# Optimization experiments

Measured on AMD Instinct MI355X. Metric: run time of the kernel, lower is better.

Reference implementation:

```python
import jax, jax.numpy as jnp
import numpy as np

# dims
B, NO, NE = 32, 100, 600          # batch, img objects, img edges
NK, KE, L = 1000, 1000, 8         # kg entities, kg edges, token len
R = 8                              # reasoning-program nodes
H, IMG, LOC = 512, 2048, 5        # hidden, img feat, loc feat
EMB, V, MID, C = 300, 10000, 512, 3000
PAD = 1


def lang_encode(tokens, embed, W, b):
    # masked mean-pool of word embeddings + projection (LanguageEncoder)
    m = (tokens != PAD).astype(jnp.float32)            # [B,N,L]
    e = embed[tokens]                                   # [B,N,L,EMB]
    pooled = (e * m[..., None]).sum(-2) / jnp.maximum(m.sum(-1, keepdims=True), 1.0)
    return jnp.tanh(pooled @ W + b)                     # [B,N,H]


def find_attn(q, k, mask, Wq, Wk, v):
    # Find module: additive attention of program-node queries over key set
    qp = q @ Wq                                         # [B,R,MID]
    kp = k @ Wk                                         # [B,N,MID]
    s = jnp.einsum('brnm,m->brn', jnp.tanh(qp[:, :, None, :] + kp[:, None, :, :]), v)
    if mask is not None:
        s = jnp.where(mask[:, None, :], s, -1e9)
    return jax.nn.softmax(s, axis=-1)                   # [B,R,N] attention maps


def setup_inputs():
    key = jax.random.key(0)
    ks = jax.random.split(key, 30)
    w = lambda i, shp: jax.random.normal(ks[i], shp, jnp.float32) * 0.05
    inp = {
        'img_feat': jax.random.normal(ks[0], (B, NO, IMG), jnp.float32),
        'img_loc': jax.random.uniform(ks[1], (B, NO, LOC), jnp.float32),
        'img_node1_id_list': jax.random.randint(ks[2], (B, NE), 0, NO),
        'img_node2_id_list': jax.random.randint(ks[3], (B, NE), 0, NO),
        'kg_entity': jax.random.randint(ks[4], (B, NK, L), 0, V),
        'kg_e1_ids_list': jax.random.randint(ks[5], (B, KE), 0, NK),
        'kg_e2_ids_list': jax.random.randint(ks[6], (B, KE), 0, NK),
        'kg_edge': jax.random.randint(ks[7], (B, KE, L), 0, V),
        'r_nodes': jax.random.randint(ks[8], (B, R, L), 0, V),
        'r_connects': jax.random.randint(ks[9], (B, R), 0, R),
        'r_type': jax.random.randint(ks[10], (B, R), 0, 3),
        'embed': w(11, (V, EMB)),
        'W_lang': w(12, (EMB, H)), 'b_lang': jnp.zeros((H,), jnp.float32),
        'W_img': w(13, (IMG, H)), 'b_img': jnp.zeros((H,), jnp.float32),
        'W_loc': w(14, (LOC, H)), 'b_loc': jnp.zeros((H,), jnp.float32),
        'W_rel': w(15, (2 * H, H)), 'b_rel': jnp.zeros((H,), jnp.float32),
        'Wq_n': w(16, (H, MID)), 'Wk_n': w(17, (H, MID)), 'v_n': w(18, (MID,)),
        'Wq_e': w(19, (H, MID)), 'Wk_e': w(20, (H, MID)), 'v_e': w(21, (MID,)),
        'W1': w(22, (H, MID)), 'b1': jnp.zeros((MID,), jnp.float32),
        'W2': w(23, (MID, C)), 'b2': jnp.zeros((C,), jnp.float32),
    }
    return inp


def reference(img_feat, img_loc, img_node1_id_list, img_node2_id_list, kg_entity,
              kg_e1_ids_list, kg_e2_ids_list, kg_edge, r_nodes, r_connects, r_type,
              embed, W_lang, b_lang, W_img, b_img, W_loc, b_loc, W_rel, b_rel,
              Wq_n, Wk_n, v_n, Wq_e, Wk_e, v_e, W1, b1, W2, b2):
    # --- image graph features ---
    img_f = img_feat @ W_img + b_img                    # [B,NO,H]
    img_node_feat = img_f + (img_loc @ W_loc + b_loc)
    n1 = jnp.take_along_axis(img_f, img_node1_id_list[..., None], axis=1)  # [B,NE,H]
    n2 = jnp.take_along_axis(img_f, img_node2_id_list[..., None], axis=1)
    img_edge_feat = jnp.concatenate([n1, n2], -1) @ W_rel + b_rel          # [B,NE,H]
    # --- kg graph features ---
    kg_node_feat = lang_encode(kg_entity, embed, W_lang, b_lang)           # [B,NK,H]
    kg_node_mask = jnp.any(kg_entity != PAD, axis=-1)                      # [B,NK]
    kg_edge_feat = lang_encode(kg_edge, embed, W_lang, b_lang)             # [B,KE,H]
    # --- reasoning-program node features ---
    r_feat = lang_encode(r_nodes, embed, W_lang, b_lang)                   # [B,R,H]
    # --- Find over nodes (img + kg entities) ---
    node_keys = jnp.concatenate([img_node_feat, kg_node_feat], axis=1)     # [B,NO+NK,H]
    node_mask = jnp.concatenate([jnp.ones((B, NO), bool), kg_node_mask], axis=1)
    all_map = find_attn(r_feat, node_keys, node_mask, Wq_n, Wk_n, v_n)     # [B,R,NO+NK]
    node_re = jnp.einsum('brn,bnh->brh', all_map, node_keys)               # grounded node feats
    # --- Find over edges (img + kg relations) ---
    edge_keys = jnp.concatenate([img_edge_feat, kg_edge_feat], axis=1)     # [B,NE+KE,H]
    edge_map = find_attn(r_feat, edge_keys, None, Wq_e, Wk_e, v_e)
    edge_ctx = jnp.einsum('brn,bnh->brh', edge_map, edge_keys)
    # --- Reason head on root program node ---
    final = node_re[:, -1] + edge_ctx[:, -1]                               # [B,H]
    return jnp.tanh(final @ W1 + b1) @ W2 + b2                             # [B,C]
```

## Files before the change

kernel.cpp:

```cpp
#include <hip/hip_runtime.h>
#include <hip/hip_bf16.h>
#include <math.h>

#define B_   32
#define NO_  100
#define NE_  600
#define NK_  1000
#define KE_  1000
#define L_   8
#define R_   8
#define H_   512
#define IMG_ 2048
#define LOC_ 5
#define EMB_ 300
#define MID_ 512
#define C_   3000
#define PAD_ 1

#define NN_  (NO_ + NK_)
#define NEK_ (NE_ + KE_)

typedef __attribute__((ext_vector_type(8))) short bf16x8;
typedef __attribute__((ext_vector_type(4))) float f32x4;

__device__ __forceinline__ float4 ldf4(const float* p) { return *(const float4*)p; }

__device__ __forceinline__ float bf2f(short s) {
    unsigned u = ((unsigned)(unsigned short)s) << 16;
    float f; __builtin_memcpy(&f, &u, 4); return f;
}
__device__ __forceinline__ short f2bf(float f) {
    unsigned u; __builtin_memcpy(&u, &f, 4);
    u = (u + 0x7fffu + ((u >> 16) & 1u)) >> 16;
    return (short)u;
}

__global__ __launch_bounds__(256) void wprep_kernel(
    const float* __restrict__ W, short* __restrict__ Wp, int K, int KS)
{
    int idx = blockIdx.x * 256 + threadIdx.x;
    int total = 4 * KS * 4 * 128;
    if (idx >= total) return;
    int nl = idx & 127;
    int kg = (idx >> 7) & 3;
    int t  = idx >> 9;
    int ks = t % KS;
    int nb = t / KS;
    int n = nb * 128 + nl;
    short o[8];
#pragma unroll
    for (int j = 0; j < 8; ++j) {
        int k = ks * 32 + kg * 8 + j;
        o[j] = (k < K) ? f2bf(W[(long)k * H_ + n]) : (short)0;
    }
    *(uint4*)&Wp[(long)idx * 8] = *(uint4*)o;
}

__global__ __launch_bounds__(256) void cvt_bf16_kernel(
    const float* __restrict__ src, short* __restrict__ dst, long n)
{
    long i = ((long)blockIdx.x * 256 + threadIdx.x) * 8;
    if (i >= n) return;
    float4 a = ldf4(src + i), b = ldf4(src + i + 4);
    short o[8] = { f2bf(a.x), f2bf(a.y), f2bf(a.z), f2bf(a.w),
                   f2bf(b.x), f2bf(b.y), f2bf(b.z), f2bf(b.w) };
    *(uint4*)&dst[i] = *(uint4*)o;
}

__global__ __launch_bounds__(256) void pool_kernel(
    const int* __restrict__ tokens, int tok_stride, int tok_off,
    const short* __restrict__ embed_bf, short* __restrict__ pooled,
    float* __restrict__ maskout, int nrows)
{
    __shared__ int   toks[32][8];
    __shared__ float rinv[32];
    int tid = threadIdx.x, base = blockIdx.x * 32;
    {
        int r = tid >> 3, t = tid & 7;
        int i = base + r;
        toks[r][t] = (i < nrows) ? tokens[tok_off + (long)i * tok_stride + t] : PAD_;
    }
    __syncthreads();
    if (tid < 32) {
        int c = 0;
#pragma unroll
        for (int t = 0; t < 8; ++t) c += (toks[tid][t] != PAD_);
        rinv[tid] = 1.0f / fmaxf((float)c, 1.0f);
        int i = base + tid;
        if (maskout && i < nrows) maskout[i] = (c > 0) ? 1.0f : 0.0f;
    }
    __syncthreads();

    for (int task = tid; task < 32 * 40; task += 256) {
        int r = task / 40, kg = task - r * 40;
        float s[8] = {0.f,0.f,0.f,0.f,0.f,0.f,0.f,0.f};
        if (kg < 38) {
#pragma unroll
            for (int t = 0; t < 8; ++t) {
                int tok = toks[r][t];
                if (tok != PAD_) {
                    bf16x8 e = *(const bf16x8*)&embed_bf[(long)tok * EMB_ + kg * 8];
#pragma unroll
                    for (int j = 0; j < 8; ++j) s[j] += bf2f(e[j]);
                }
            }
        }
        float iv = rinv[r];
        short o[8];
#pragma unroll
        for (int j = 0; j < 8; ++j) {
            float v = s[j] * iv;
            if (kg == 37 && j >= 4) v = 0.f;
            o[j] = f2bf(v);
        }
        *(uint4*)&pooled[(long)(base + r) * 320 + kg * 8] = *(uint4*)o;
    }
}

template<int OUTF32>
__global__ __launch_bounds__(256) void keys_gemm_kernel(
    const short* __restrict__ A, const short* __restrict__ Wp,
    const float* __restrict__ bias,
    void* __restrict__ out, int rows_per_b, long out_bstride, long out_roff,
    float* __restrict__ unused, int nrows)
{
    const int KS = 10;
    __shared__ __align__(16) short As[4096];
    __shared__ __align__(16) short Bs[4096];
    int tid = threadIdx.x;
    int m0 = blockIdx.x * 128, nb = blockIdx.y, n0 = nb * 128;
    int w = tid >> 6, l = tid & 63, wr = w >> 1, wc = w & 1;
    int sr = tid >> 1, sh = tid & 1;
    long arow_off = (long)(m0 + sr) * 320;
    const short* wslab = Wp + (long)nb * KS * 4096;

    uint4 av0, av1, bv0, bv1;
    auto loadA = [&](int ks) {
        const short* p = A + arow_off + ks * 32 + sh * 16;
        av0 = *(const uint4*)p;
        av1 = *(const uint4*)(p + 8);
    };
    auto loadB = [&](int ks) {
        const uint4* p = (const uint4*)(wslab + (long)ks * 4096 + tid * 16);
        bv0 = p[0]; bv1 = p[1];
    };

    f32x4 acc[4][4];
#pragma unroll
    for (int m = 0; m < 4; ++m)
#pragma unroll
        for (int n = 0; n < 4; ++n)
#pragma unroll
            for (int k = 0; k < 4; ++k) acc[m][n][k] = 0.f;

    int kg = l >> 4, li = l & 15;
    loadA(0); loadB(0);
    for (int ks = 0; ks < KS; ++ks) {
        __syncthreads();
        *(uint4*)&As[(sh * 2) * 1024 + sr * 8]     = av0;
        *(uint4*)&As[(sh * 2 + 1) * 1024 + sr * 8] = av1;
        *(uint4*)&Bs[tid * 16]     = bv0;
        *(uint4*)&Bs[tid * 16 + 8] = bv1;
        __syncthreads();
        if (ks + 1 < KS) { loadA(ks + 1); loadB(ks + 1); }
        bf16x8 af[4], bfr[4];
#pragma unroll
        for (int m = 0; m < 4; ++m)
            af[m] = *(const bf16x8*)&As[kg * 1024 + (wr * 64 + m * 16 + li) * 8];
#pragma unroll
        for (int n = 0; n < 4; ++n)
            bfr[n] = *(const bf16x8*)&Bs[kg * 1024 + (wc * 64 + n * 16 + li) * 8];
#pragma unroll
        for (int m = 0; m < 4; ++m)
#pragma unroll
            for (int n = 0; n < 4; ++n)
                acc[m][n] = __builtin_amdgcn_mfma_f32_16x16x32_bf16(af[m], bfr[n], acc[m][n], 0, 0, 0);
    }

    int jrow4 = (l >> 4) * 4;
    float bv[4];
#pragma unroll
    for (int n = 0; n < 4; ++n) bv[n] = bias[n0 + wc * 64 + n * 16 + li];
#pragma unroll
    for (int m = 0; m < 4; ++m)
#pragma unroll
        for (int j = 0; j < 4; ++j) {
            int i = m0 + wr * 64 + m * 16 + jrow4 + j;
            if (i >= nrows) continue;
            int b = i / rows_per_b, k = i - b * rows_per_b;
#pragma unroll
            for (int n = 0; n < 4; ++n) {
                int col = n0 + wc * 64 + n * 16 + li;
                float val = tanhf(acc[m][n][j] + bv[n]);
                long idx = (long)b * out_bstride + out_roff + (long)k * H_ + col;
                if (OUTF32) ((float*)out)[idx] = val;
                else        ((short*)out)[idx] = f2bf(val);
            }
        }
    (void)unused;
}

template<int AV, int EP>
__global__ __launch_bounds__(256) void mfma_gemm_kernel(
    const short* __restrict__ A, int lda, const short* __restrict__ Wp, int KS,
    const int* __restrict__ id1, const int* __restrict__ id2,
    const short* __restrict__ Agather,
    const float* __restrict__ bias, const float* __restrict__ bias2,
    const float* __restrict__ loc, const float* __restrict__ Wloc,
    const float* __restrict__ qp, const float* __restrict__ vvec,
    short* __restrict__ out0, short* __restrict__ out1,
    float* __restrict__ sout, int Nrows, int Mtot)
{
    __shared__ __align__(16) short As[4096];
    __shared__ __align__(16) short Bs[4096];
    int tid = threadIdx.x;
    int m0 = blockIdx.x * 128, nb = blockIdx.y, n0 = nb * 128;
    int w = tid >> 6, l = tid & 63, wr = w >> 1, wc = w & 1;
    int sr = tid >> 1, sh = tid & 1;

    long arow_off = 0; int r1 = 0, r2 = 0;
    if (AV == 0) {
        arow_off = (long)(m0 + sr) * lda;
    } else {
        int i = m0 + sr;
        int b = i / NE_;
        r1 = b * NO_ + id1[i];
        r2 = b * NO_ + id2[i];
    }
    const short* wslab = Wp + (long)nb * KS * 4096;

    uint4 av0, av1, bv0, bv1;
    auto loadA = [&](int ks) {
        const short* p;
        if (AV == 0) p = A + arow_off + ks * 32 + sh * 16;
        else {
            int kk = ks * 32;
            int row = (kk < 512) ? r1 : r2;
            p = Agather + (long)row * 512 + (kk & 511) + sh * 16;
        }
        av0 = *(const uint4*)p;
        av1 = *(const uint4*)(p + 8);
    };
    auto loadB = [&](int ks) {
        const uint4* p = (const uint4*)(wslab + (long)ks * 4096 + tid * 16);
        bv0 = p[0]; bv1 = p[1];
    };

    f32x4 acc[4][4];
#pragma unroll
    for (int m = 0; m < 4; ++m)
#pragma unroll
        for (int n = 0; n < 4; ++n)
#pragma unroll
            for (int k = 0; k < 4; ++k) acc[m][n][k] = 0.f;

    int kg = l >> 4, li = l & 15;
    loadA(0); loadB(0);
    for (int ks = 0; ks < KS; ++ks) {
        __syncthreads();
        *(uint4*)&As[(sh * 2) * 1024 + sr * 8]     = av0;
        *(uint4*)&As[(sh * 2 + 1) * 1024 + sr * 8] = av1;
        *(uint4*)&Bs[tid * 16]     = bv0;
        *(uint4*)&Bs[tid * 16 + 8] = bv1;
        __syncthreads();
        if (ks + 1 < KS) { loadA(ks + 1); loadB(ks + 1); }
        bf16x8 af[4], bfr[4];
#pragma unroll
        for (int m = 0; m < 4; ++m)
            af[m] = *(const bf16x8*)&As[kg * 1024 + (wr * 64 + m * 16 + li) * 8];
#pragma unroll
        for (int n = 0; n < 4; ++n)
            bfr[n] = *(const bf16x8*)&Bs[kg * 1024 + (wc * 64 + n * 16 + li) * 8];
#pragma unroll
        for (int m = 0; m < 4; ++m)
#pragma unroll
            for (int n = 0; n < 4; ++n)
                acc[m][n] = __builtin_amdgcn_mfma_f32_16x16x32_bf16(af[m], bfr[n], acc[m][n], 0, 0, 0);
    }

    int jrow4 = (l >> 4) * 4;
    if (EP == 0) {
        float bi[4], bl[4], wl[4][5];
#pragma unroll
        for (int n = 0; n < 4; ++n) {
            int col = n0 + wc * 64 + n * 16 + li;
            bi[n] = bias[col]; bl[n] = bias2[col];
#pragma unroll
            for (int j5 = 0; j5 < 5; ++j5) wl[n][j5] = Wloc[j5 * H_ + col];
        }
#pragma unroll
        for (int m = 0; m < 4; ++m)
#pragma unroll
            for (int j = 0; j < 4; ++j) {
                int row = m0 + wr * 64 + m * 16 + jrow4 + j;
                int b = row / NO_, o = row - b * NO_;
                float lv[5];
#pragma unroll
                for (int j5 = 0; j5 < 5; ++j5) lv[j5] = loc[(long)row * 5 + j5];
#pragma unroll
                for (int n = 0; n < 4; ++n) {
                    int col = n0 + wc * 64 + n * 16 + li;
                    float val = acc[m][n][j] + bi[n];
                    out0[(long)row * H_ + col] = f2bf(val);
                    float nk = val + bl[n];
#pragma unroll
                    for (int j5 = 0; j5 < 5; ++j5) nk = fmaf(lv[j5], wl[n][j5], nk);
                    out1[((long)b * NN_ + o) * H_ + col] = f2bf(nk);
                }
            }
    } else if (EP == 1) {
        float bi[4];
#pragma unroll
        for (int n = 0; n < 4; ++n) bi[n] = bias[n0 + wc * 64 + n * 16 + li];
#pragma unroll
        for (int m = 0; m < 4; ++m)
#pragma unroll
            for (int j = 0; j < 4; ++j) {
                int row = m0 + wr * 64 + m * 16 + jrow4 + j;
                int b = row / NE_, e = row - b * NE_;
#pragma unroll
                for (int n = 0; n < 4; ++n) {
                    int col = n0 + wc * 64 + n * 16 + li;
                    out0[((long)b * NEK_ + e) * H_ + col] = f2bf(acc[m][n][j] + bi[n]);
                }
            }
    } else {
        float vv[4];
        int cols[4];
#pragma unroll
        for (int n = 0; n < 4; ++n) {
            cols[n] = n0 + wc * 64 + n * 16 + li;
            vv[n] = vvec[cols[n]];
        }
        int slot = nb * 2 + wc;
#pragma unroll
        for (int m = 0; m < 4; ++m)
#pragma unroll
            for (int j = 0; j < 4; ++j) {
                int row = m0 + wr * 64 + m * 16 + jrow4 + j;
                int b = row / Nrows;
                const float* qpb = qp + (long)b * H_;
                float p = 0.f;
#pragma unroll
                for (int n = 0; n < 4; ++n)
                    p += tanhf(qpb[cols[n]] + acc[m][n][j]) * vv[n];
                p += __shfl_xor(p, 1); p += __shfl_xor(p, 2);
                p += __shfl_xor(p, 4); p += __shfl_xor(p, 8);
                if (li == 0) sout[(long)slot * Mtot + row] = p;
            }
    }
}

__global__ __launch_bounds__(256) void softmax_w_kernel(
    const float* __restrict__ sp_n, const float* __restrict__ sp_e,
    const float* __restrict__ maskbuf, float* __restrict__ wn, float* __restrict__ we)
{
    __shared__ float sw[NEK_];
    __shared__ float red[256];
    int b = blockIdx.x, tid = threadIdx.x, set = blockIdx.y;
    const float* sp = set ? sp_e : sp_n;
    float* wout = set ? we : wn;
    int N = set ? NEK_ : NN_;
    long Mtot = set ? (long)B_ * NEK_ : (long)B_ * NN_;

    float lmax = -3.0e38f;
    for (int n = tid; n < N; n += 256) {
        long row = (long)b * N + n;
        float x = 0.f;
#pragma unroll
        for (int s = 0; s < 8; ++s) x += sp[(long)s * Mtot + row];
        if (!set && n >= NO_ && maskbuf[(long)b * NK_ + (n - NO_)] == 0.f) x = -1e30f;
        sw[n] = x;
        lmax = fmaxf(lmax, x);
    }
    red[tid] = lmax; __syncthreads();
    for (int st = 128; st > 0; st >>= 1) {
        if (tid < st) red[tid] = fmaxf(red[tid], red[tid + st]);
        __syncthreads();
    }
    float mx = red[0]; __syncthreads();

    float lsum = 0.f;
    for (int n = tid; n < N; n += 256) {
        float e = expf(sw[n] - mx);
        sw[n] = e;
        lsum += e;
    }
    red[tid] = lsum; __syncthreads();
    for (int st = 128; st > 0; st >>= 1) {
        if (tid < st) red[tid] += red[tid + st];
        __syncthreads();
    }
    float invZ = 1.0f / red[0];
    __syncthreads();
    for (int n = tid; n < N; n += 256)
        wout[(long)b * N + n] = sw[n] * invZ;
}

template<int SP>
__global__ __launch_bounds__(256) void wsum_kernel(
    const float* __restrict__ w, const short* __restrict__ keys,
    float* __restrict__ partial, int N)
{
    __shared__ float red[4][512];
    int b = blockIdx.x, sp = blockIdx.y, tid = threadIdx.x;
    int c8 = (tid & 63) * 8, rsub = tid >> 6;
    int per = (N + SP - 1) / SP;
    int n0 = sp * per, n1 = min(n0 + per, N);
    float acc[8] = {0.f,0.f,0.f,0.f,0.f,0.f,0.f,0.f};
    for (int n = n0 + rsub; n < n1; n += 4) {
        float wv = w[(long)b * N + n];
        bf16x8 k = *(const bf16x8*)&keys[((long)b * N + n) * H_ + c8];
#pragma unroll
        for (int j = 0; j < 8; ++j) acc[j] = fmaf(wv, bf2f(k[j]), acc[j]);
    }
    *(float4*)&red[rsub][c8]     = *(float4*)acc;
    *(float4*)&red[rsub][c8 + 4] = *(float4*)(acc + 4);
    __syncthreads();
    if (rsub == 0) {
        float o[8];
#pragma unroll
        for (int j = 0; j < 8; ++j)
            o[j] = red[0][c8 + j] + red[1][c8 + j] + red[2][c8 + j] + red[3][c8 + j];
        float* op = &partial[((long)sp * B_ + b) * H_ + c8];
        *(float4*)op       = *(float4*)o;
        *(float4*)(op + 4) = *(float4*)(o + 4);
    }
}

__global__ __launch_bounds__(256) void fin_reduce_kernel(
    const float* __restrict__ pn, const float* __restrict__ pe, float* __restrict__ fin)
{
    int i = blockIdx.x * 256 + threadIdx.x;
    float s = 0.f;
#pragma unroll
    for (int sp = 0; sp < 16; ++sp)
        s += pn[(long)sp * B_ * H_ + i] + pe[(long)sp * B_ * H_ + i];
    fin[i] = s;
}

template<int E, int CHUNK>
__global__ __launch_bounds__(256) void kmatvec_kernel(
    const float* __restrict__ in, const float* __restrict__ Wa,
    const float* __restrict__ Wb, float* __restrict__ pa,
    float* __restrict__ pb, int C)
{
    __shared__ float ins[32 * CHUNK];
    int tid = threadIdx.x;
    int ks = blockIdx.y, k0 = ks * CHUNK;
    const float* W   = (blockIdx.z == 0) ? Wa : Wb;
    float* partial   = (blockIdx.z == 0) ? pa : pb;
    for (int t = tid; t < 32 * CHUNK; t += 256) {
        int b = t / CHUNK, k = t - b * CHUNK;
        ins[t] = in[(long)b * E + k0 + k];
    }
    __syncthreads();
    int c = blockIdx.x * 256 + tid;
    if (c >= C) return;
    float acc[32];
#pragma unroll
    for (int b = 0; b < 32; ++b) acc[b] = 0.f;
    for (int k = 0; k < CHUNK; ++k) {
        float wv = W[(long)(k0 + k) * C + c];
#pragma unroll
        for (int b = 0; b < 32; ++b)
            acc[b] = fmaf(ins[b * CHUNK + k], wv, acc[b]);
    }
#pragma unroll
    for (int b = 0; b < 32; ++b)
        partial[((long)ks * 32 + b) * C + c] = acc[b];
}

template<int ACT, int KS>
__global__ __launch_bounds__(256) void kreduce_kernel(
    const float* __restrict__ pa, const float* __restrict__ pb,
    const float* __restrict__ biasa, const float* __restrict__ biasb,
    float* __restrict__ oa, float* __restrict__ ob, int C)
{
    int set = blockIdx.y;
    const float* p    = set ? pb : pa;
    const float* bias = set ? biasb : biasa;
    float* o          = set ? ob : oa;
    long i = (long)blockIdx.x * 256 + threadIdx.x;
    if (i >= 32L * C) return;
    int c = (int)(i % C);
    float s = bias ? bias[c] : 0.f;
#pragma unroll
    for (int ks = 0; ks < KS; ++ks) s += p[(long)ks * 32 * C + i];
    o[i] = (ACT == 1) ? tanhf(s) : s;
}

extern "C" void kernel_launch(void* const* d_in, const int* in_sizes, int n_in,
                              void* d_out, int out_size, void* d_ws, size_t ws_size,
                              hipStream_t stream)
{
    (void)in_sizes; (void)n_in; (void)out_size; (void)ws_size;

    const float* img_feat  = (const float*)d_in[0];
    const float* img_loc   = (const float*)d_in[1];
    const int*   id1       = (const int*)d_in[2];
    const int*   id2       = (const int*)d_in[3];
    const int*   kg_entity = (const int*)d_in[4];
    const int*   kg_edge   = (const int*)d_in[7];
    const int*   r_nodes   = (const int*)d_in[8];
    const float* embed     = (const float*)d_in[11];
    const float* W_lang    = (const float*)d_in[12];
    const float* b_lang    = (const float*)d_in[13];
    const float* W_img     = (const float*)d_in[14];
    const float* b_img     = (const float*)d_in[15];
    const float* W_loc     = (const float*)d_in[16];
    const float* b_loc     = (const float*)d_in[17];
    const float* W_rel     = (const float*)d_in[18];
    const float* b_rel     = (const float*)d_in[19];
    const float* Wq_n      = (const float*)d_in[20];
    const float* Wk_n      = (const float*)d_in[21];
    const float* v_n       = (const float*)d_in[22];
    const float* Wq_e      = (const float*)d_in[23];
    const float* Wk_e      = (const float*)d_in[24];
    const float* v_e       = (const float*)d_in[25];
    const float* W1        = (const float*)d_in[26];
    const float* b1        = (const float*)d_in[27];
    const float* W2        = (const float*)d_in[28];
    const float* b2        = (const float*)d_in[29];
    float* out = (float*)d_out;

    char* ws = (char*)d_ws;
    size_t off = 0;
    auto allocS = [&](size_t n) { short* p = (short*)(ws + off); off += ((n * 2 + 255) & ~255ULL); return p; };
    auto allocF = [&](size_t n) { float* p = (float*)(ws + off); off += ((n * 4 + 255) & ~255ULL); return p; };

    short* img_feat_bf = allocS((size_t)B_ * NO_ * IMG_);
    short* embed_bf    = allocS((size_t)10000 * EMB_ + 16);
    short* Wp_img      = allocS((size_t)4 * 64 * 4096);
    short* Wp_rel      = allocS((size_t)4 * 32 * 4096);
    short* Wp_kn       = allocS((size_t)4 * 16 * 4096);
    short* Wp_ke       = allocS((size_t)4 * 16 * 4096);
    short* Wp_lang     = allocS((size_t)4 * 10 * 4096);
    short* img_f_bf    = allocS((size_t)B_ * NO_ * H_);
    short* node_keys   = allocS((size_t)B_ * NN_ * H_);
    short* edge_keys   = allocS((size_t)B_ * NEK_ * H_);
    short* pooled_n    = allocS((size_t)B_ * NK_ * 320);
    short* pooled_e    = allocS((size_t)B_ * KE_ * 320);
    short* pooled_r    = allocS((size_t)128 * 320);
    float* rfeat   = allocF((size_t)B_ * H_);
    float* qp_n    = allocF((size_t)B_ * H_);
    float* qp_e    = allocF((size_t)B_ * H_);
    float* mask_kg = allocF((size_t)B_ * NK_);
    float* sp_n    = allocF((size_t)8 * B_ * NN_);
    float* sp_e    = allocF((size_t)8 * B_ * NEK_);
    float* wn      = allocF((size_t)B_ * NN_);
    float* we      = allocF((size_t)B_ * NEK_);
    float* pn      = allocF((size_t)16 * B_ * H_);
    float* pe      = allocF((size_t)16 * B_ * H_);
    float* fin     = allocF((size_t)B_ * H_);
    float* hid     = allocF((size_t)B_ * H_);
    float* pq_n    = allocF((size_t)16 * B_ * MID_);
    float* pq_e    = allocF((size_t)16 * B_ * MID_);
    float* ph1     = allocF((size_t)16 * B_ * MID_);
    float* ph2     = allocF((size_t)16 * B_ * C_);

    cvt_bf16_kernel<<<(B_ * NO_ * IMG_ / 8 + 255) / 256, 256, 0, stream>>>(
        img_feat, img_feat_bf, (long)B_ * NO_ * IMG_);
    cvt_bf16_kernel<<<(10000 * EMB_ / 8 + 255) / 256, 256, 0, stream>>>(
        embed, embed_bf, (long)10000 * EMB_);
    wprep_kernel<<<512, 256, 0, stream>>>(W_img,  Wp_img,  IMG_, 64);
    wprep_kernel<<<256, 256, 0, stream>>>(W_rel,  Wp_rel,  1024, 32);
    wprep_kernel<<<128, 256, 0, stream>>>(Wk_n,   Wp_kn,   512,  16);
    wprep_kernel<<<128, 256, 0, stream>>>(Wk_e,   Wp_ke,   512,  16);
    wprep_kernel<<< 80, 256, 0, stream>>>(W_lang, Wp_lang, EMB_, 10);

    pool_kernel<<<B_ * NK_ / 32, 256, 0, stream>>>(
        kg_entity, L_, 0, embed_bf, pooled_n, mask_kg, B_ * NK_);
    pool_kernel<<<B_ * KE_ / 32, 256, 0, stream>>>(
        kg_edge, L_, 0, embed_bf, pooled_e, nullptr, B_ * KE_);
    pool_kernel<<<4, 256, 0, stream>>>(
        r_nodes, R_ * L_, (R_ - 1) * L_, embed_bf, pooled_r, nullptr, B_);

    keys_gemm_kernel<0><<<dim3(B_ * NK_ / 128, 4), 256, 0, stream>>>(
        pooled_n, Wp_lang, b_lang, node_keys, NK_, (long)NN_ * H_, (long)NO_ * H_,
        nullptr, B_ * NK_);
    keys_gemm_kernel<0><<<dim3(B_ * KE_ / 128, 4), 256, 0, stream>>>(
        pooled_e, Wp_lang, b_lang, edge_keys, KE_, (long)NEK_ * H_, (long)NE_ * H_,
        nullptr, B_ * KE_);
    keys_gemm_kernel<1><<<dim3(1, 4), 256, 0, stream>>>(
        pooled_r, Wp_lang, b_lang, rfeat, 1, (long)H_, 0L, nullptr, B_);

    kmatvec_kernel<H_, 32><<<dim3(2, 16, 2), 256, 0, stream>>>(
        rfeat, Wq_n, Wq_e, pq_n, pq_e, MID_);
    kreduce_kernel<0, 16><<<dim3(B_ * MID_ / 256, 2), 256, 0, stream>>>(
        pq_n, pq_e, nullptr, nullptr, qp_n, qp_e, MID_);

    mfma_gemm_kernel<0, 0><<<dim3(B_ * NO_ / 128, 4), 256, 0, stream>>>(
        img_feat_bf, IMG_, Wp_img, 64, nullptr, nullptr, nullptr,
        b_img, b_loc, img_loc, W_loc, nullptr, nullptr,
        img_f_bf, node_keys, nullptr, 0, 0);
    mfma_gemm_kernel<2, 1><<<dim3(B_ * NE_ / 128, 4), 256, 0, stream>>>(
        nullptr, 0, Wp_rel, 32, id1, id2, img_f_bf,
        b_rel, nullptr, nullptr, nullptr, nullptr, nullptr,
        edge_keys, nullptr, nullptr, 0, 0);

    mfma_gemm_kernel<0, 2><<<dim3(B_ * NN_ / 128, 4), 256, 0, stream>>>(
        node_keys, H_, Wp_kn, 16, nullptr, nullptr, nullptr,
        nullptr, nullptr, nullptr, nullptr, qp_n, v_n,
        nullptr, nullptr, sp_n, NN_, B_ * NN_);
    mfma_gemm_kernel<0, 2><<<dim3(B_ * NEK_ / 128, 4), 256, 0, stream>>>(
        edge_keys, H_, Wp_ke, 16, nullptr, nullptr, nullptr,
        nullptr, nullptr, nullptr, nullptr, qp_e, v_e,
        nullptr, nullptr, sp_e, NEK_, B_ * NEK_);

    softmax_w_kernel<<<dim3(B_, 2), 256, 0, stream>>>(sp_n, sp_e, mask_kg, wn, we);
    wsum_kernel<16><<<dim3(B_, 16), 256, 0, stream>>>(wn, node_keys, pn, NN_);
    wsum_kernel<16><<<dim3(B_, 16), 256, 0, stream>>>(we, edge_keys, pe, NEK_);
    fin_reduce_kernel<<<B_ * H_ / 256, 256, 0, stream>>>(pn, pe, fin);

    kmatvec_kernel<H_, 32><<<dim3(2, 16, 1), 256, 0, stream>>>(
        fin, W1, W1, ph1, ph1, MID_);
    kreduce_kernel<1, 16><<<dim3(B_ * MID_ / 256, 1), 256, 0, stream>>>(
        ph1, ph1, b1, b1, hid, hid, MID_);
    kmatvec_kernel<MID_, 32><<<dim3((C_ + 255) / 256, 16, 1), 256, 0, stream>>>(
        hid, W2, W2, ph2, ph2, C_);
    kreduce_kernel<0, 16><<<dim3((B_ * C_ + 255) / 256, 1), 256, 0, stream>>>(
        ph2, ph2, b2, b2, out, out, C_);
}
```

Before: 447.1 us.

## Loop all N-blocks inside one GEMM block and pad LDS k-groups

```diff
diff --git a/kernel.cpp b/kernel.cpp
--- a/kernel.cpp
+++ b/kernel.cpp
@@ -19,6 +19,7 @@
 
 #define NN_  (NO_ + NK_)
 #define NEK_ (NE_ + KE_)
+#define KGP_ 1040
 
 typedef __attribute__((ext_vector_type(8))) short bf16x8;
 typedef __attribute__((ext_vector_type(4))) float f32x4;
@@ -122,17 +123,17 @@
     const short* __restrict__ A, const short* __restrict__ Wp,
     const float* __restrict__ bias,
     void* __restrict__ out, int rows_per_b, long out_bstride, long out_roff,
-    float* __restrict__ unused, int nrows)
+    int nrows)
 {
     const int KS = 10;
-    __shared__ __align__(16) short As[4096];
-    __shared__ __align__(16) short Bs[4096];
+    __shared__ __align__(16) short As[4 * KGP_];
+    __shared__ __align__(16) short Bs[4 * KGP_];
     int tid = threadIdx.x;
-    int m0 = blockIdx.x * 128, nb = blockIdx.y, n0 = nb * 128;
+    int m0 = blockIdx.x * 128;
     int w = tid >> 6, l = tid & 63, wr = w >> 1, wc = w & 1;
     int sr = tid >> 1, sh = tid & 1;
     long arow_off = (long)(m0 + sr) * 320;
-    const short* wslab = Wp + (long)nb * KS * 4096;
+    int bkg = tid >> 6, brem = (tid & 63) * 16;
 
     uint4 av0, av1, bv0, bv1;
     auto loadA = [&](int ks) {
@@ -140,69 +141,73 @@
         av0 = *(const uint4*)p;
         av1 = *(const uint4*)(p + 8);
     };
-    auto loadB = [&](int ks) {
-        const uint4* p = (const uint4*)(wslab + (long)ks * 4096 + tid * 16);
+    auto loadB = [&](int nb, int ks) {
+        const uint4* p = (const uint4*)(Wp + ((long)nb * KS + ks) * 4096 + tid * 16);
         bv0 = p[0]; bv1 = p[1];
     };
 
-    f32x4 acc[4][4];
-#pragma unroll
-    for (int m = 0; m < 4; ++m)
-#pragma unroll
-        for (int n = 0; n < 4; ++n)
-#pragma unroll
-            for (int k = 0; k < 4; ++k) acc[m][n][k] = 0.f;
-
     int kg = l >> 4, li = l & 15;
-    loadA(0); loadB(0);
-    for (int ks = 0; ks < KS; ++ks) {
-        __syncthreads();
-        *(uint4*)&As[(sh * 2) * 1024 + sr * 8]     = av0;
-        *(uint4*)&As[(sh * 2 + 1) * 1024 + sr * 8] = av1;
-        *(uint4*)&Bs[tid * 16]     = bv0;
-        *(uint4*)&Bs[tid * 16 + 8] = bv1;
-        __syncthreads();
-        if (ks + 1 < KS) { loadA(ks + 1); loadB(ks + 1); }
-        bf16x8 af[4], bfr[4];
+    int jrow4 = (l >> 4) * 4;
+    loadA(0); loadB(0, 0);
+    for (int nb = 0; nb < 4; ++nb) {
+        int n0 = nb * 128;
+        f32x4 acc[4][4];
 #pragma unroll
         for (int m = 0; m < 4; ++m)
-            af[m] = *(const bf16x8*)&As[kg * 1024 + (wr * 64 + m * 16 + li) * 8];
-#pragma unroll
-        for (int n = 0; n < 4; ++n)
-            bfr[n] = *(const bf16x8*)&Bs[kg * 1024 + (wc * 64 + n * 16 + li) * 8];
+#pragma unroll
+            for (int n = 0; n < 4; ++n)
+#pragma unroll
+                for (int k = 0; k < 4; ++k) acc[m][n][k] = 0.f;
+
+        for (int ks = 0; ks < KS; ++ks) {
+            __syncthreads();
+            *(uint4*)&As[(sh * 2) * KGP_ + sr * 8]     = av0;
+            *(uint4*)&As[(sh * 2 + 1) * KGP_ + sr * 8] = av1;
+            *(uint4*)&Bs[bkg * KGP_ + brem]     = bv0;
+            *(uint4*)&Bs[bkg * KGP_ + brem + 8] = bv1;
+            __syncthreads();
+            int ks2 = ks + 1, nb2 = nb;
+            if (ks2 == KS) { ks2 = 0; ++nb2; }
+            if (nb2 < 4) { loadA(ks2); loadB(nb2, ks2); }
+            bf16x8 af[4], bfr[4];
+#pragma unroll
+            for (int m = 0; m < 4; ++m)
+                af[m] = *(const bf16x8*)&As[kg * KGP_ + (wr * 64 + m * 16 + li) * 8];
+#pragma unroll
+            for (int n = 0; n < 4; ++n)
+                bfr[n] = *(const bf16x8*)&Bs[kg * KGP_ + (wc * 64 + n * 16 + li) * 8];
+#pragma unroll
+            for (int m = 0; m < 4; ++m)
+#pragma unroll
+                for (int n = 0; n < 4; ++n)
+                    acc[m][n] = __builtin_amdgcn_mfma_f32_16x16x32_bf16(af[m], bfr[n], acc[m][n], 0, 0, 0);
+        }
+
+        float bv[4];
+#pragma unroll
+        for (int n = 0; n < 4; ++n) bv[n] = bias[n0 + wc * 64 + n * 16 + li];
 #pragma unroll
         for (int m = 0; m < 4; ++m)
 #pragma unroll
-            for (int n = 0; n < 4; ++n)
-                acc[m][n] = __builtin_amdgcn_mfma_f32_16x16x32_bf16(af[m], bfr[n], acc[m][n], 0, 0, 0);
-    }
-
-    int jrow4 = (l >> 4) * 4;
-    float bv[4];
-#pragma unroll
-    for (int n = 0; n < 4; ++n) bv[n] = bias[n0 + wc * 64 + n * 16 + li];
-#pragma unroll
-    for (int m = 0; m < 4; ++m)
-#pragma unroll
-        for (int j = 0; j < 4; ++j) {
-            int i = m0 + wr * 64 + m * 16 + jrow4 + j;
-            if (i >= nrows) continue;
-            int b = i / rows_per_b, k = i - b * rows_per_b;
-#pragma unroll
-            for (int n = 0; n < 4; ++n) {
-                int col = n0 + wc * 64 + n * 16 + li;
-                float val = tanhf(acc[m][n][j] + bv[n]);
-                long idx = (long)b * out_bstride + out_roff + (long)k * H_ + col;
-                if (OUTF32) ((float*)out)[idx] = val;
-                else        ((short*)out)[idx] = f2bf(val);
+            for (int j = 0; j < 4; ++j) {
+                int i = m0 + wr * 64 + m * 16 + jrow4 + j;
+                if (i >= nrows) continue;
+                int b = i / rows_per_b, k = i - b * rows_per_b;
+#pragma unroll
+                for (int n = 0; n < 4; ++n) {
+                    int col = n0 + wc * 64 + n * 16 + li;
+                    float val = tanhf(acc[m][n][j] + bv[n]);
+                    long idx = (long)b * out_bstride + out_roff + (long)k * H_ + col;
+                    if (OUTF32) ((float*)out)[idx] = val;
+                    else        ((short*)out)[idx] = f2bf(val);
+                }
             }
-        }
-    (void)unused;
-}
-
-template<int AV, int EP>
+    }
+}
+
+template<int AV, int EP, int KS, int NBL>
 __global__ __launch_bounds__(256) void mfma_gemm_kernel(
-    const short* __restrict__ A, int lda, const short* __restrict__ Wp, int KS,
+    const short* __restrict__ A, int lda, const short* __restrict__ Wp,
     const int* __restrict__ id1, const int* __restrict__ id2,
     const short* __restrict__ Agather,
     const float* __restrict__ bias, const float* __restrict__ bias2,
@@ -211,12 +216,14 @@
     short* __restrict__ out0, short* __restrict__ out1,
     float* __restrict__ sout, int Nrows, int Mtot)
 {
-    __shared__ __align__(16) short As[4096];
-    __shared__ __align__(16) short Bs[4096];
+    __shared__ __align__(16) short As[4 * KGP_];
+    __shared__ __align__(16) short Bs[4 * KGP_];
     int tid = threadIdx.x;
-    int m0 = blockIdx.x * 128, nb = blockIdx.y, n0 = nb * 128;
+    int m0 = blockIdx.x * 128;
+    int nb0 = blockIdx.y * NBL;
     int w = tid >> 6, l = tid & 63, wr = w >> 1, wc = w & 1;
     int sr = tid >> 1, sh = tid & 1;
+    int bkg = tid >> 6, brem = (tid & 63) * 16;
 
     long arow_off = 0; int r1 = 0, r2 = 0;
     if (AV == 0) {
@@ -227,7 +234,6 @@
         r1 = b * NO_ + id1[i];
         r2 = b * NO_ + id2[i];
     }
-    const short* wslab = Wp + (long)nb * KS * 4096;
 
     uint4 av0, av1, bv0, bv1;
     auto loadA = [&](int ks) {
@@ -241,113 +247,119 @@
         av0 = *(const uint4*)p;
         av1 = *(const uint4*)(p + 8);
     };
-    auto loadB = [&](int ks) {
-        const uint4* p = (const uint4*)(wslab + (long)ks * 4096 + tid * 16);
+    auto loadB = [&](int nb, int ks) {
+        const uint4* p = (const uint4*)(Wp + ((long)nb * KS + ks) * 4096 + tid * 16);
         bv0 = p[0]; bv1 = p[1];
     };
 
-    f32x4 acc[4][4];
-#pragma unroll
-    for (int m = 0; m < 4; ++m)
-#pragma unroll
-        for (int n = 0; n < 4; ++n)
-#pragma unroll
-            for (int k = 0; k < 4; ++k) acc[m][n][k] = 0.f;
-
     int kg = l >> 4, li = l & 15;
-    loadA(0); loadB(0);
-    for (int ks = 0; ks < KS; ++ks) {
-        __syncthreads();
-        *(uint4*)&As[(sh * 2) * 1024 + sr * 8]     = av0;
-        *(uint4*)&As[(sh * 2 + 1) * 1024 + sr * 8] = av1;
-        *(uint4*)&Bs[tid * 16]     = bv0;
-        *(uint4*)&Bs[tid * 16 + 8] = bv1;
-        __syncthreads();
-        if (ks + 1 < KS) { loadA(ks + 1); loadB(ks + 1); }
-        bf16x8 af[4], bfr[4];
+    int jrow4 = (l >> 4) * 4;
+    loadA(0); loadB(nb0, 0);
+    for (int it = 0; it < NBL; ++it) {
+        int nb = nb0 + it;
+        int n0 = nb * 128;
+        f32x4 acc[4][4];
 #pragma unroll
         for (int m = 0; m < 4; ++m)
-            af[m] = *(const bf16x8*)&As[kg * 1024 + (wr * 64 + m * 16 + li) * 8];
-#pragma unroll
-        for (int n = 0; n < 4; ++n)
-            bfr[n] = *(const bf16x8*)&Bs[kg * 1024 + (wc * 64 + n * 16 + li) * 8];
-#pragma unroll
-        for (int m = 0; m < 4; ++m)
 #pragma unroll
             for (int n = 0; n < 4; ++n)
-                acc[m][n] = __builtin_amdgcn_mfma_f32_16x16x32_bf16(af[m], bfr[n], acc[m][n], 0, 0, 0);
-    }
-
-    int jrow4 = (l >> 4) * 4;
-    if (EP == 0) {
-        float bi[4], bl[4], wl[4][5];
-#pragma unroll
-        for (int n = 0; n < 4; ++n) {
-            int col = n0 + wc * 64 + n * 16 + li;
-            bi[n] = bias[col]; bl[n] = bias2[col];
-#pragma unroll
-            for (int j5 = 0; j5 < 5; ++j5) wl[n][j5] = Wloc[j5 * H_ + col];
+#pragma unroll
+                for (int k = 0; k < 4; ++k) acc[m][n][k] = 0.f;
+
+        for (int ks = 0; ks < KS; ++ks) {
+            __syncthreads();
+            *(uint4*)&As[(sh * 2) * KGP_ + sr * 8]     = av0;
+            *(uint4*)&As[(sh * 2 + 1) * KGP_ + sr * 8] = av1;
+            *(uint4*)&Bs[bkg * KGP_ + brem]     = bv0;
+            *(uint4*)&Bs[bkg * KGP_ + brem + 8] = bv1;
+            __syncthreads();
+            int ks2 = ks + 1, nb2 = nb;
+            if (ks2 == KS) { ks2 = 0; ++nb2; }
+            if (nb2 < nb0 + NBL) { loadA(ks2); loadB(nb2, ks2); }
+            bf16x8 af[4], bfr[4];
+#pragma unroll
+            for (int m = 0; m < 4; ++m)
+                af[m] = *(const bf16x8*)&As[kg * KGP_ + (wr * 64 + m * 16 + li) * 8];
+#pragma unroll
+            for (int n = 0; n < 4; ++n)
+                bfr[n] = *(const bf16x8*)&Bs[kg * KGP_ + (wc * 64 + n * 16 + li) * 8];
+#pragma unroll
+            for (int m = 0; m < 4; ++m)
+#pragma unroll
+                for (int n = 0; n < 4; ++n)
+                    acc[m][n] = __builtin_amdgcn_mfma_f32_16x16x32_bf16(af[m], bfr[n], acc[m][n], 0, 0, 0);
         }
-#pragma unroll
-        for (int m = 0; m < 4; ++m)
-#pragma unroll
-            for (int j = 0; j < 4; ++j) {
-                int row = m0 + wr * 64 + m * 16 + jrow4 + j;
-                int b = row / NO_, o = row - b * NO_;
-                float lv[5];
-#pragma unroll
-                for (int j5 = 0; j5 < 5; ++j5) lv[j5] = loc[(long)row * 5 + j5];
-#pragma unroll
-                for (int n = 0; n < 4; ++n) {
-                    int col = n0 + wc * 64 + n * 16 + li;
-                    float val = acc[m][n][j] + bi[n];
-                    out0[(long)row * H_ + col] = f2bf(val);
-                    float nk = val + bl[n];
-#pragma unroll
-                    for (int j5 = 0; j5 < 5; ++j5) nk = fmaf(lv[j5], wl[n][j5], nk);
-                    out1[((long)b * NN_ + o) * H_ + col] = f2bf(nk);
+
+        if (EP == 0) {
+            float bi[4], bl[4], wl[4][5];
+#pragma unroll
+            for (int n = 0; n < 4; ++n) {
+                int col = n0 + wc * 64 + n * 16 + li;
+                bi[n] = bias[col]; bl[n] = bias2[col];
+#pragma unroll
+                for (int j5 = 0; j5 < 5; ++j5) wl[n][j5] = Wloc[j5 * H_ + col];
+            }
+#pragma unroll
+            for (int m = 0; m < 4; ++m)
+#pragma unroll
+                for (int j = 0; j < 4; ++j) {
+                    int row = m0 + wr * 64 + m * 16 + jrow4 + j;
+                    int b = row / NO_, o = row - b * NO_;
+                    float lv[5];
+#pragma unroll
+                    for (int j5 = 0; j5 < 5; ++j5) lv[j5] = loc[(long)row * 5 + j5];
+#pragma unroll
+                    for (int n = 0; n < 4; ++n) {
+                        int col = n0 + wc * 64 + n * 16 + li;
+                        float val = acc[m][n][j] + bi[n];
+                        out0[(long)row * H_ + col] = f2bf(val);
+                        float nk = val + bl[n];
+#pragma unroll
+                        for (int j5 = 0; j5 < 5; ++j5) nk = fmaf(lv[j5], wl[n][j5], nk);
+                        out1[((long)b * NN_ + o) * H_ + col] = f2bf(nk);
+                    }
                 }
+        } else if (EP == 1) {
+            float bi[4];
+#pragma unroll
+            for (int n = 0; n < 4; ++n) bi[n] = bias[n0 + wc * 64 + n * 16 + li];
+#pragma unroll
+            for (int m = 0; m < 4; ++m)
+#pragma unroll
+                for (int j = 0; j < 4; ++j) {
+                    int row = m0 + wr * 64 + m * 16 + jrow4 + j;
+                    int b = row / NE_, e = row - b * NE_;
+#pragma unroll
+                    for (int n = 0; n < 4; ++n) {
+                        int col = n0 + wc * 64 + n * 16 + li;
+                        out0[((long)b * NEK_ + e) * H_ + col] = f2bf(acc[m][n][j] + bi[n]);
+                    }
+                }
+        } else {
+            float vv[4];
+            int cols[4];
+#pragma unroll
+            for (int n = 0; n < 4; ++n) {
+                cols[n] = n0 + wc * 64 + n * 16 + li;
+                vv[n] = vvec[cols[n]];
             }
-    } else if (EP == 1) {
-        float bi[4];
-#pragma unroll
-        for (int n = 0; n < 4; ++n) bi[n] = bias[n0 + wc * 64 + n * 16 + li];
-#pragma unroll
-        for (int m = 0; m < 4; ++m)
-#pragma unroll
-            for (int j = 0; j < 4; ++j) {
-                int row = m0 + wr * 64 + m * 16 + jrow4 + j;
-                int b = row / NE_, e = row - b * NE_;
-#pragma unroll
-                for (int n = 0; n < 4; ++n) {
-                    int col = n0 + wc * 64 + n * 16 + li;
-                    out0[((long)b * NEK_ + e) * H_ + col] = f2bf(acc[m][n][j] + bi[n]);
+            int slot = nb * 2 + wc;
+#pragma unroll
+            for (int m = 0; m < 4; ++m)
+#pragma unroll
+                for (int j = 0; j < 4; ++j) {
+                    int row = m0 + wr * 64 + m * 16 + jrow4 + j;
+                    int b = row / Nrows;
+                    const float* qpb = qp + (long)b * H_;
+                    float p = 0.f;
+#pragma unroll
+                    for (int n = 0; n < 4; ++n)
+                        p += tanhf(qpb[cols[n]] + acc[m][n][j]) * vv[n];
+                    p += __shfl_xor(p, 1); p += __shfl_xor(p, 2);
+                    p += __shfl_xor(p, 4); p += __shfl_xor(p, 8);
+                    if (li == 0) sout[(long)slot * Mtot + row] = p;
                 }
-            }
-    } else {
-        float vv[4];
-        int cols[4];
-#pragma unroll
-        for (int n = 0; n < 4; ++n) {
-            cols[n] = n0 + wc * 64 + n * 16 + li;
-            vv[n] = vvec[cols[n]];
         }
-        int slot = nb * 2 + wc;
-#pragma unroll
-        for (int m = 0; m < 4; ++m)
-#pragma unroll
-            for (int j = 0; j < 4; ++j) {
-                int row = m0 + wr * 64 + m * 16 + jrow4 + j;
-                int b = row / Nrows;
-                const float* qpb = qp + (long)b * H_;
-                float p = 0.f;
-#pragma unroll
-                for (int n = 0; n < 4; ++n)
-                    p += tanhf(qpb[cols[n]] + acc[m][n][j]) * vv[n];
-                p += __shfl_xor(p, 1); p += __shfl_xor(p, 2);
-                p += __shfl_xor(p, 4); p += __shfl_xor(p, 8);
-                if (li == 0) sout[(long)slot * Mtot + row] = p;
-            }
     }
 }
 
@@ -576,35 +588,35 @@
     pool_kernel<<<4, 256, 0, stream>>>(
         r_nodes, R_ * L_, (R_ - 1) * L_, embed_bf, pooled_r, nullptr, B_);
 
-    keys_gemm_kernel<0><<<dim3(B_ * NK_ / 128, 4), 256, 0, stream>>>(
+    keys_gemm_kernel<0><<<B_ * NK_ / 128, 256, 0, stream>>>(
         pooled_n, Wp_lang, b_lang, node_keys, NK_, (long)NN_ * H_, (long)NO_ * H_,
-        nullptr, B_ * NK_);
-    keys_gemm_kernel<0><<<dim3(B_ * KE_ / 128, 4), 256, 0, stream>>>(
+        B_ * NK_);
+    keys_gemm_kernel<0><<<B_ * KE_ / 128, 256, 0, stream>>>(
         pooled_e, Wp_lang, b_lang, edge_keys, KE_, (long)NEK_ * H_, (long)NE_ * H_,
-        nullptr, B_ * KE_);
-    keys_gemm_kernel<1><<<dim3(1, 4), 256, 0, stream>>>(
-        pooled_r, Wp_lang, b_lang, rfeat, 1, (long)H_, 0L, nullptr, B_);
+        B_ * KE_);
+    keys_gemm_kernel<1><<<1, 256, 0, stream>>>(
+        pooled_r, Wp_lang, b_lang, rfeat, 1, (long)H_, 0L, B_);
 
     kmatvec_kernel<H_, 32><<<dim3(2, 16, 2), 256, 0, stream>>>(
         rfeat, Wq_n, Wq_e, pq_n, pq_e, MID_);
     kreduce_kernel<0, 16><<<dim3(B_ * MID_ / 256, 2), 256, 0, stream>>>(
         pq_n, pq_e, nullptr, nullptr, qp_n, qp_e, MID_);
 
-    mfma_gemm_kernel<0, 0><<<dim3(B_ * NO_ / 128, 4), 256, 0, stream>>>(
-        img_feat_bf, IMG_, Wp_img, 64, nullptr, nullptr, nullptr,
+    mfma_gemm_kernel<0, 0, 64, 1><<<dim3(B_ * NO_ / 128, 4), 256, 0, stream>>>(
+        img_feat_bf, IMG_, Wp_img, nullptr, nullptr, nullptr,
         b_img, b_loc, img_loc, W_loc, nullptr, nullptr,
         img_f_bf, node_keys, nullptr, 0, 0);
-    mfma_gemm_kernel<2, 1><<<dim3(B_ * NE_ / 128, 4), 256, 0, stream>>>(
-        nullptr, 0, Wp_rel, 32, id1, id2, img_f_bf,
+    mfma_gemm_kernel<2, 1, 32, 1><<<dim3(B_ * NE_ / 128, 4), 256, 0, stream>>>(
+        nullptr, 0, Wp_rel, id1, id2, img_f_bf,
         b_rel, nullptr, nullptr, nullptr, nullptr, nullptr,
         edge_keys, nullptr, nullptr, 0, 0);
 
-    mfma_gemm_kernel<0, 2><<<dim3(B_ * NN_ / 128, 4), 256, 0, stream>>>(
-        node_keys, H_, Wp_kn, 16, nullptr, nullptr, nullptr,
+    mfma_gemm_kernel<0, 2, 16, 4><<<B_ * NN_ / 128, 256, 0, stream>>>(
+        node_keys, H_, Wp_kn, nullptr, nullptr, nullptr,
         nullptr, nullptr, nullptr, nullptr, qp_n, v_n,
         nullptr, nullptr, sp_n, NN_, B_ * NN_);
-    mfma_gemm_kernel<0, 2><<<dim3(B_ * NEK_ / 128, 4), 256, 0, stream>>>(
-        edge_keys, H_, Wp_ke, 16, nullptr, nullptr, nullptr,
+    mfma_gemm_kernel<0, 2, 16, 4><<<B_ * NEK_ / 128, 256, 0, stream>>>(
+        edge_keys, H_, Wp_ke, nullptr, nullptr, nullptr,
         nullptr, nullptr, nullptr, nullptr, qp_e, v_e,
         nullptr, nullptr, sp_e, NEK_, B_ * NEK_);
 
```

Result: slower. 572.0 us (+27.9%).

## Double-buffer GEMM tiles in LDS using direct global-to-LDS loads

Applied to the files above, without the earlier changes.

```diff
diff --git a/kernel.cpp b/kernel.cpp
--- a/kernel.cpp
+++ b/kernel.cpp
@@ -35,6 +35,12 @@
     return (short)u;
 }
 
+__device__ __forceinline__ void gload16(const void* g, void* l) {
+    __builtin_amdgcn_global_load_lds(
+        (__attribute__((address_space(1))) void*)(g),
+        (__attribute__((address_space(3))) void*)(l), 16, 0, 0);
+}
+
 __global__ __launch_bounds__(256) void wprep_kernel(
     const float* __restrict__ W, short* __restrict__ Wp, int K, int KS)
 {
@@ -122,28 +128,27 @@
     const short* __restrict__ A, const short* __restrict__ Wp,
     const float* __restrict__ bias,
     void* __restrict__ out, int rows_per_b, long out_bstride, long out_roff,
-    float* __restrict__ unused, int nrows)
+    int nrows)
 {
     const int KS = 10;
-    __shared__ __align__(16) short As[4096];
-    __shared__ __align__(16) short Bs[4096];
+    __shared__ __align__(16) short As[2 * 4096];
+    __shared__ __align__(16) short Bs[2 * 4096];
     int tid = threadIdx.x;
     int m0 = blockIdx.x * 128, nb = blockIdx.y, n0 = nb * 128;
     int w = tid >> 6, l = tid & 63, wr = w >> 1, wc = w & 1;
-    int sr = tid >> 1, sh = tid & 1;
-    long arow_off = (long)(m0 + sr) * 320;
     const short* wslab = Wp + (long)nb * KS * 4096;
 
-    uint4 av0, av1, bv0, bv1;
-    auto loadA = [&](int ks) {
-        const short* p = A + arow_off + ks * 32 + sh * 16;
-        av0 = *(const uint4*)p;
-        av1 = *(const uint4*)(p + 8);
+    auto stage = [&](int buf, int ks) {
+        short* Ad = As + buf * 4096 + w * 1024;
+        short* Bd = Bs + buf * 4096 + w * 1024;
+        const short* bsrc = wslab + (long)ks * 4096 + w * 1024 + l * 8;
+#pragma unroll
+        for (int i = 0; i < 2; ++i) {
+            const short* ga = A + (long)(m0 + i * 64 + l) * 320 + ks * 32 + w * 8;
+            gload16(ga, Ad + i * 512);
+            gload16(bsrc + i * 512, Bd + i * 512);
+        }
     };
-    auto loadB = [&](int ks) {
-        const uint4* p = (const uint4*)(wslab + (long)ks * 4096 + tid * 16);
-        bv0 = p[0]; bv1 = p[1];
-    };
 
     f32x4 acc[4][4];
 #pragma unroll
@@ -154,27 +159,25 @@
             for (int k = 0; k < 4; ++k) acc[m][n][k] = 0.f;
 
     int kg = l >> 4, li = l & 15;
-    loadA(0); loadB(0);
+    stage(0, 0);
+    __syncthreads();
+    int buf = 0;
     for (int ks = 0; ks < KS; ++ks) {
-        __syncthreads();
-        *(uint4*)&As[(sh * 2) * 1024 + sr * 8]     = av0;
-        *(uint4*)&As[(sh * 2 + 1) * 1024 + sr * 8] = av1;
-        *(uint4*)&Bs[tid * 16]     = bv0;
-        *(uint4*)&Bs[tid * 16 + 8] = bv1;
-        __syncthreads();
-        if (ks + 1 < KS) { loadA(ks + 1); loadB(ks + 1); }
+        if (ks + 1 < KS) stage(buf ^ 1, ks + 1);
         bf16x8 af[4], bfr[4];
 #pragma unroll
         for (int m = 0; m < 4; ++m)
-            af[m] = *(const bf16x8*)&As[kg * 1024 + (wr * 64 + m * 16 + li) * 8];
+            af[m] = *(const bf16x8*)&As[buf * 4096 + kg * 1024 + (wr * 64 + m * 16 + li) * 8];
 #pragma unroll
         for (int n = 0; n < 4; ++n)
-            bfr[n] = *(const bf16x8*)&Bs[kg * 1024 + (wc * 64 + n * 16 + li) * 8];
+            bfr[n] = *(const bf16x8*)&Bs[buf * 4096 + kg * 1024 + (wc * 64 + n * 16 + li) * 8];
 #pragma unroll
         for (int m = 0; m < 4; ++m)
 #pragma unroll
             for (int n = 0; n < 4; ++n)
                 acc[m][n] = __builtin_amdgcn_mfma_f32_16x16x32_bf16(af[m], bfr[n], acc[m][n], 0, 0, 0);
+        __syncthreads();
+        buf ^= 1;
     }
 
     int jrow4 = (l >> 4) * 4;
@@ -197,12 +200,11 @@
                 else        ((short*)out)[idx] = f2bf(val);
             }
         }
-    (void)unused;
-}
-
-template<int AV, int EP>
+}
+
+template<int AV, int EP, int KS>
 __global__ __launch_bounds__(256) void mfma_gemm_kernel(
-    const short* __restrict__ A, int lda, const short* __restrict__ Wp, int KS,
+    const short* __restrict__ A, int lda, const short* __restrict__ Wp,
     const int* __restrict__ id1, const int* __restrict__ id2,
     const short* __restrict__ Agather,
     const float* __restrict__ bias, const float* __restrict__ bias2,
@@ -211,40 +213,42 @@
     short* __restrict__ out0, short* __restrict__ out1,
     float* __restrict__ sout, int Nrows, int Mtot)
 {
-    __shared__ __align__(16) short As[4096];
-    __shared__ __align__(16) short Bs[4096];
+    __shared__ __align__(16) short As[2 * 4096];
+    __shared__ __align__(16) short Bs[2 * 4096];
     int tid = threadIdx.x;
     int m0 = blockIdx.x * 128, nb = blockIdx.y, n0 = nb * 128;
     int w = tid >> 6, l = tid & 63, wr = w >> 1, wc = w & 1;
-    int sr = tid >> 1, sh = tid & 1;
-
-    long arow_off = 0; int r1 = 0, r2 = 0;
-    if (AV == 0) {
-        arow_off = (long)(m0 + sr) * lda;
-    } else {
-        int i = m0 + sr;
-        int b = i / NE_;
-        r1 = b * NO_ + id1[i];
-        r2 = b * NO_ + id2[i];
+
+    int r1[2], r2[2];
+    if (AV == 2) {
+#pragma unroll
+        for (int i = 0; i < 2; ++i) {
+            int row = m0 + i * 64 + l;
+            int b = row / NE_;
+            r1[i] = b * NO_ + id1[row];
+            r2[i] = b * NO_ + id2[row];
+        }
     }
     const short* wslab = Wp + (long)nb * KS * 4096;
 
-    uint4 av0, av1, bv0, bv1;
-    auto loadA = [&](int ks) {
-        const short* p;
-        if (AV == 0) p = A + arow_off + ks * 32 + sh * 16;
-        else {
-            int kk = ks * 32;
-            int row = (kk < 512) ? r1 : r2;
-            p = Agather + (long)row * 512 + (kk & 511) + sh * 16;
-        }
-        av0 = *(const uint4*)p;
-        av1 = *(const uint4*)(p + 8);
+    auto stage = [&](int buf, int ks) {
+        short* Ad = As + buf * 4096 + w * 1024;
+        short* Bd = Bs + buf * 4096 + w * 1024;
+        const short* bsrc = wslab + (long)ks * 4096 + w * 1024 + l * 8;
+#pragma unroll
+        for (int i = 0; i < 2; ++i) {
+            const short* ga;
+            if (AV == 0) {
+                ga = A + (long)(m0 + i * 64 + l) * lda + ks * 32 + w * 8;
+            } else {
+                int kk = ks * 32;
+                int row = (kk < 512) ? r1[i] : r2[i];
+                ga = Agather + (long)row * 512 + (kk & 511) + w * 8;
+            }
+            gload16(ga, Ad + i * 512);
+            gload16(bsrc + i * 512, Bd + i * 512);
+        }
     };
-    auto loadB = [&](int ks) {
-        const uint4* p = (const uint4*)(wslab + (long)ks * 4096 + tid * 16);
-        bv0 = p[0]; bv1 = p[1];
-    };
 
     f32x4 acc[4][4];
 #pragma unroll
@@ -255,27 +259,25 @@
             for (int k = 0; k < 4; ++k) acc[m][n][k] = 0.f;
 
     int kg = l >> 4, li = l & 15;
-    loadA(0); loadB(0);
+    stage(0, 0);
+    __syncthreads();
+    int buf = 0;
     for (int ks = 0; ks < KS; ++ks) {
-        __syncthreads();
-        *(uint4*)&As[(sh * 2) * 1024 + sr * 8]     = av0;
-        *(uint4*)&As[(sh * 2 + 1) * 1024 + sr * 8] = av1;
-        *(uint4*)&Bs[tid * 16]     = bv0;
-        *(uint4*)&Bs[tid * 16 + 8] = bv1;
-        __syncthreads();
-        if (ks + 1 < KS) { loadA(ks + 1); loadB(ks + 1); }
+        if (ks + 1 < KS) stage(buf ^ 1, ks + 1);
         bf16x8 af[4], bfr[4];
 #pragma unroll
         for (int m = 0; m < 4; ++m)
-            af[m] = *(const bf16x8*)&As[kg * 1024 + (wr * 64 + m * 16 + li) * 8];
+            af[m] = *(const bf16x8*)&As[buf * 4096 + kg * 1024 + (wr * 64 + m * 16 + li) * 8];
 #pragma unroll
         for (int n = 0; n < 4; ++n)
-            bfr[n] = *(const bf16x8*)&Bs[kg * 1024 + (wc * 64 + n * 16 + li) * 8];
+            bfr[n] = *(const bf16x8*)&Bs[buf * 4096 + kg * 1024 + (wc * 64 + n * 16 + li) * 8];
 #pragma unroll
         for (int m = 0; m < 4; ++m)
 #pragma unroll
             for (int n = 0; n < 4; ++n)
                 acc[m][n] = __builtin_amdgcn_mfma_f32_16x16x32_bf16(af[m], bfr[n], acc[m][n], 0, 0, 0);
+        __syncthreads();
+        buf ^= 1;
     }
 
     int jrow4 = (l >> 4) * 4;
@@ -578,33 +580,33 @@
 
     keys_gemm_kernel<0><<<dim3(B_ * NK_ / 128, 4), 256, 0, stream>>>(
         pooled_n, Wp_lang, b_lang, node_keys, NK_, (long)NN_ * H_, (long)NO_ * H_,
-        nullptr, B_ * NK_);
+        B_ * NK_);
     keys_gemm_kernel<0><<<dim3(B_ * KE_ / 128, 4), 256, 0, stream>>>(
         pooled_e, Wp_lang, b_lang, edge_keys, KE_, (long)NEK_ * H_, (long)NE_ * H_,
-        nullptr, B_ * KE_);
+        B_ * KE_);
     keys_gemm_kernel<1><<<dim3(1, 4), 256, 0, stream>>>(
-        pooled_r, Wp_lang, b_lang, rfeat, 1, (long)H_, 0L, nullptr, B_);
+        pooled_r, Wp_lang, b_lang, rfeat, 1, (long)H_, 0L, B_);
 
     kmatvec_kernel<H_, 32><<<dim3(2, 16, 2), 256, 0, stream>>>(
         rfeat, Wq_n, Wq_e, pq_n, pq_e, MID_);
     kreduce_kernel<0, 16><<<dim3(B_ * MID_ / 256, 2), 256, 0, stream>>>(
         pq_n, pq_e, nullptr, nullptr, qp_n, qp_e, MID_);
 
-    mfma_gemm_kernel<0, 0><<<dim3(B_ * NO_ / 128, 4), 256, 0, stream>>>(
-        img_feat_bf, IMG_, Wp_img, 64, nullptr, nullptr, nullptr,
+    mfma_gemm_kernel<0, 0, 64><<<dim3(B_ * NO_ / 128, 4), 256, 0, stream>>>(
+        img_feat_bf, IMG_, Wp_img, nullptr, nullptr, nullptr,
         b_img, b_loc, img_loc, W_loc, nullptr, nullptr,
         img_f_bf, node_keys, nullptr, 0, 0);
-    mfma_gemm_kernel<2, 1><<<dim3(B_ * NE_ / 128, 4), 256, 0, stream>>>(
-        nullptr, 0, Wp_rel, 32, id1, id2, img_f_bf,
+    mfma_gemm_kernel<2, 1, 32><<<dim3(B_ * NE_ / 128, 4), 256, 0, stream>>>(
+        nullptr, 0, Wp_rel, id1, id2, img_f_bf,
         b_rel, nullptr, nullptr, nullptr, nullptr, nullptr,
         edge_keys, nullptr, nullptr, 0, 0);
 
-    mfma_gemm_kernel<0, 2><<<dim3(B_ * NN_ / 128, 4), 256, 0, stream>>>(
-        node_keys, H_, Wp_kn, 16, nullptr, nullptr, nullptr,
+    mfma_gemm_kernel<0, 2, 16><<<dim3(B_ * NN_ / 128, 4), 256, 0, stream>>>(
+        node_keys, H_, Wp_kn, nullptr, nullptr, nullptr,
         nullptr, nullptr, nullptr, nullptr, qp_n, v_n,
         nullptr, nullptr, sp_n, NN_, B_ * NN_);
-    mfma_gemm_kernel<0, 2><<<dim3(B_ * NEK_ / 128, 4), 256, 0, stream>>>(
-        edge_keys, H_, Wp_ke, 16, nullptr, nullptr, nullptr,
+    mfma_gemm_kernel<0, 2, 16><<<dim3(B_ * NEK_ / 128, 4), 256, 0, stream>>>(
+        edge_keys, H_, Wp_ke, nullptr, nullptr, nullptr,
         nullptr, nullptr, nullptr, nullptr, qp_e, v_e,
         nullptr, nullptr, sp_e, NEK_, B_ * NEK_);
 
```

New measurement: 516.3 us. 15.5% more time.
